# Kernel tuning notes

Measured on AMD Instinct MI355X. Metric: run time of the kernel, lower is better.

## Reference

```python
import jax, jax.numpy as jnp
import numpy as np

B, N, D = 8, 2048, 768
H = 12
HD = D // H
W = 16          # window_size
HOP = 8         # hop_size
GB = N // 2 + 1   # global freq bins = 1025
LB = W // 2 + 1   # local freq bins = 9
NW = (N - W) // HOP + 1  # num windows = 255
EPS_LN = 1e-5


def setup_inputs() -> dict:
    key = jax.random.key(0)
    ks = jax.random.split(key, 12)
    s = 0.02
    return {
        "x": jax.random.normal(ks[0], (B, N, D), dtype=jnp.float32),
        "base_filter_global": jnp.ones((H, GB, 1), jnp.float32),
        "base_filter_local": jnp.ones((H, LB, 1), jnp.float32),
        "modrelu_bias_global": jnp.full((H, GB, 1), -0.1, jnp.float32),
        "modrelu_bias_local": jnp.full((H, LB, 1), -0.1, jnp.float32),
        "w1g": jax.random.normal(ks[1], (D, D), jnp.float32) * s,
        "b1g": jnp.zeros((D,), jnp.float32),
        "w2g": jax.random.normal(ks[2], (D, H * GB), jnp.float32) * s,
        "b2g": jnp.zeros((H * GB,), jnp.float32),
        "w1l": jax.random.normal(ks[3], (D, D), jnp.float32) * s,
        "b1l": jnp.zeros((D,), jnp.float32),
        "w2l": jax.random.normal(ks[4], (D, H * LB), jnp.float32) * s,
        "b2l": jnp.zeros((H * LB,), jnp.float32),
        "fusion_w": jax.random.normal(ks[5], (2,), jnp.float32) * 0.5,
        "ln_gamma": jnp.ones((D,), jnp.float32),
        "ln_beta": jnp.zeros((D,), jnp.float32),
    }


def _modrelu(z, bias):
    # modReLU: ReLU(|z| + b) * z / |z|  (|z| clamped at 1e-6 in denominator)
    a = jnp.abs(z)
    return z * (jax.nn.relu(a + bias) / jnp.maximum(a, 1e-6))


def _hann(w):
    # torch.hann_window default (periodic=True)
    n = jnp.arange(w, dtype=jnp.float32)
    return 0.5 * (1.0 - jnp.cos(2.0 * jnp.pi * n / w))


def reference(x, base_filter_global, base_filter_local, modrelu_bias_global,
              modrelu_bias_local, w1g, b1g, w2g, b2g, w1l, b1l, w2l, b2l,
              fusion_w, ln_gamma, ln_beta):
    b, n, d = x.shape
    x_heads = x.reshape(b, n, H, HD).transpose(0, 2, 1, 3)  # (B,H,N,hd)

    # ---- global branch ----
    Fg = jnp.fft.rfft(x_heads, axis=2, norm='ortho')  # (B,H,GB,hd) complex
    ctx = x.mean(axis=1)  # (B,D)
    mg = jnp.tanh(jax.nn.gelu(ctx @ w1g + b1g, approximate=False) @ w2g + b2g)
    mg = mg.reshape(b, H, GB, 1)
    Fg = Fg * (base_filter_global[None] + mg)
    Fg = _modrelu(Fg, modrelu_bias_global[None])
    x_global = jnp.fft.irfft(Fg, n=n, axis=2, norm='ortho')  # (B,H,N,hd)

    # ---- local (STFT) branch ----
    idx = jnp.arange(NW)[:, None] * HOP + jnp.arange(W)[None, :]  # (NW,W)
    x_win = x_heads[:, :, idx, :]  # (B,H,NW,W,hd)
    w = _hann(W)[None, None, None, :, None]
    x_win = x_win * w
    Fl = jnp.fft.rfft(x_win, axis=3, norm='ortho')  # (B,H,NW,LB,hd)
    ml = jnp.tanh(jax.nn.gelu(ctx @ w1l + b1l, approximate=False) @ w2l + b2l)
    ml = ml.reshape(b, H, 1, LB, 1)
    Fl = Fl * (base_filter_local[None, :, None] + ml)
    Fl = _modrelu(Fl, modrelu_bias_local[None, :, None])
    x_lwin = jnp.fft.irfft(Fl, n=W, axis=3, norm='ortho') * w  # (B,H,NW,W,hd)

    # vectorized overlap-add
    flat_idx = idx.reshape(-1)  # (NW*W,)
    x_local = jnp.zeros((b, H, n, HD), x.dtype).at[:, :, flat_idx, :].add(
        x_lwin.reshape(b, H, NW * W, HD))

    # ---- fuse + residual + layernorm ----
    fused = x_global * fusion_w[0] + x_local * fusion_w[1]  # Linear(2,1,bias=False)
    x_out = fused.transpose(0, 2, 1, 3).reshape(b, n, d)
    y = x + x_out  # dropout is identity at p=0 / eval
    mu = y.mean(axis=-1, keepdims=True)
    var = y.var(axis=-1, keepdims=True)
    return (y - mu) / jnp.sqrt(var + EPS_LN) * ln_gamma + ln_beta
```

## Files before the change

kernel.cpp:

```cpp
#include <hip/hip_runtime.h>
#include <math.h>

#define B_  8
#define N_  2048
#define D_  768
#define H_  12
#define HD_ 64
#define GB_ 1025
#define LB_ 9
#define NW_ 255

#define CBX(i) ((i) + ((i) >> 4))
#define TWX(i) ((i) + ((i) >> 4))

#define C1_ 0.92387953251128674f
#define S1_ 0.38268343236508978f
#define R2_ 0.70710678118654752f

#define FBF(i,k,wr,wi) { const float ar=yr[i],ai=yi[i],br=yr[k],bi=yi[k]; \
  yr[i]=ar+br; yi[i]=ai+bi; const float dr=ar-br, di=ai-bi; \
  yr[k]=fmaf(dr,wr,-(di*(wi))); yi[k]=fmaf(dr,wi,di*(wr)); }
#define FBF1(i,k) { const float ar=yr[i],ai=yi[i],br=yr[k],bi=yi[k]; \
  yr[i]=ar+br; yi[i]=ai+bi; yr[k]=ar-br; yi[k]=ai-bi; }
#define FBFmi(i,k) { const float ar=yr[i],ai=yi[i],br=yr[k],bi=yi[k]; \
  yr[i]=ar+br; yi[i]=ai+bi; yr[k]=ai-bi; yi[k]=br-ar; }

#define IBF(i,k,wr,wi) { const float br=yr[k],bi=yi[k]; \
  const float tr=fmaf(br,wr,-(bi*(wi))), ti=fmaf(br,wi,bi*(wr)); \
  yr[k]=yr[i]-tr; yi[k]=yi[i]-ti; yr[i]+=tr; yi[i]+=ti; }
#define IBF1(i,k) { const float tr=yr[k], ti=yi[k]; \
  yr[k]=yr[i]-tr; yi[k]=yi[i]-ti; yr[i]+=tr; yi[i]+=ti; }
#define IBFpi(i,k) { const float tr=-yi[k], ti=yr[k]; \
  yr[k]=yr[i]-tr; yi[k]=yi[i]-ti; yr[i]+=tr; yi[i]+=ti; }

__device__ __forceinline__ float2 cmulf(float2 a, float2 b) {
  return make_float2(fmaf(a.x, b.x, -(a.y*b.y)), fmaf(a.x, b.y, a.y*b.x));
}
__device__ __forceinline__ float2 csqf(float2 a){ return make_float2(fmaf(a.x,a.x,-(a.y*a.y)), 2.0f*a.x*a.y); }

__device__ __forceinline__ float4 dadd(float4 a, float4 b){ return make_float4(a.x+b.x,a.y+b.y,a.z+b.z,a.w+b.w); }
__device__ __forceinline__ float4 dsub(float4 a, float4 b){ return make_float4(a.x-b.x,a.y-b.y,a.z-b.z,a.w-b.w); }
__device__ __forceinline__ float4 dmul(float4 a, float2 w){
  return make_float4(fmaf(a.x,w.x,-(a.y*w.y)), fmaf(a.x,w.y,a.y*w.x),
                     fmaf(a.z,w.x,-(a.w*w.y)), fmaf(a.z,w.y,a.w*w.x));
}
__device__ __forceinline__ float4 dmulc(float4 a, float2 w){
  return make_float4(fmaf(a.x,w.x,a.y*w.y), fmaf(a.y,w.x,-(a.x*w.y)),
                     fmaf(a.z,w.x,a.w*w.y), fmaf(a.w,w.x,-(a.z*w.y)));
}
__device__ __forceinline__ float4 dmuli(float4 a){
  return make_float4(a.y, -a.x, a.w, -a.z);
}
__device__ __forceinline__ float4 dmulpi(float4 a){
  return make_float4(-a.y, a.x, -a.w, a.z);
}

__device__ __forceinline__ void mr2(float& ar, float& ai, float filt, float bias){
  ar *= filt; ai *= filt;
  const float a = __builtin_amdgcn_sqrtf(fmaf(ar,ar,ai*ai));
  const float s = fmaxf(a + bias, 0.0f) * __builtin_amdgcn_rcpf(fmaxf(a, 1e-6f));
  ar *= s; ai *= s;
}
__device__ __forceinline__ void mr1(float& v, float filt, float bias){
  v *= filt;
  const float a = fabsf(v);
  v *= fmaxf(a + bias, 0.0f) * __builtin_amdgcn_rcpf(fmaxf(a, 1e-6f));
}

template<int S, int L>
__device__ __forceinline__ void fft_trip_fwd(float4* cb, const float2* tw, int j) {
  const int r    = j & (S-1);
  const int base = r + ((j >> L) << (L+3));
  float4 v[8];
  #pragma unroll
  for (int k = 0; k < 8; ++k) v[k] = cb[CBX(base + S*k)];
  const float2 w = tw[TWX(r * (256/S))];
  const float2 c8 = make_float2(R2_, -R2_);
  float2 W1[4];
  W1[0] = w;
  W1[1] = cmulf(w, c8);
  W1[2] = make_float2(w.y, -w.x);
  W1[3] = make_float2(W1[1].y, -W1[1].x);
  #pragma unroll
  for (int k = 0; k < 4; ++k) {
    const float4 u = v[k], t = v[k+4];
    v[k]   = dadd(u, t);
    v[k+4] = dmul(dsub(u, t), W1[k]);
  }
  const float2 w2  = csqf(w);
  const float2 w2i = make_float2(w2.y, -w2.x);
  {
    float4 d;
    d = dsub(v[0], v[2]); v[0] = dadd(v[0], v[2]); v[2] = dmul(d, w2);
    d = dsub(v[1], v[3]); v[1] = dadd(v[1], v[3]); v[3] = dmul(d, w2i);
    d = dsub(v[4], v[6]); v[4] = dadd(v[4], v[6]); v[6] = dmul(d, w2);
    d = dsub(v[5], v[7]); v[5] = dadd(v[5], v[7]); v[7] = dmul(d, w2i);
  }
  const float2 w4 = csqf(w2);
  #pragma unroll
  for (int k = 0; k < 8; k += 2) {
    const float4 d = dsub(v[k], v[k+1]);
    v[k]   = dadd(v[k], v[k+1]);
    v[k+1] = dmul(d, w4);
  }
  #pragma unroll
  for (int k = 0; k < 8; ++k) cb[CBX(base + S*k)] = v[k];
}

__device__ __forceinline__ void fft_trip4_fwd(float4* cb, int j) {
  const int base = j << 3;
  float4 v[8];
  #pragma unroll
  for (int k = 0; k < 8; ++k) v[k] = cb[CBX(base + k)];
  float4 d;
  d = dsub(v[0], v[2]); v[0] = dadd(v[0], v[2]); v[2] = d;
  d = dsub(v[1], v[3]); v[1] = dadd(v[1], v[3]); v[3] = dmuli(d);
  d = dsub(v[4], v[6]); v[4] = dadd(v[4], v[6]); v[6] = d;
  d = dsub(v[5], v[7]); v[5] = dadd(v[5], v[7]); v[7] = dmuli(d);
  #pragma unroll
  for (int k = 0; k < 8; k += 2) {
    d = dsub(v[k], v[k+1]);
    v[k]   = dadd(v[k], v[k+1]);
    v[k+1] = d;
  }
  #pragma unroll
  for (int k = 0; k < 8; ++k) cb[CBX(base + k)] = v[k];
}

__device__ __forceinline__ void fft_trip1_inv(float4* cb, int j) {
  const int base = j << 3;
  float4 v[8];
  #pragma unroll
  for (int k = 0; k < 8; ++k) v[k] = cb[CBX(base + k)];
  #pragma unroll
  for (int k = 0; k < 8; k += 2) {
    const float4 t = v[k+1];
    v[k+1] = dsub(v[k], t);
    v[k]   = dadd(v[k], t);
  }
  {
    float4 t;
    t = v[2];          v[2] = dsub(v[0], t); v[0] = dadd(v[0], t);
    t = dmulpi(v[3]);  v[3] = dsub(v[1], t); v[1] = dadd(v[1], t);
    t = v[6];          v[6] = dsub(v[4], t); v[4] = dadd(v[4], t);
    t = dmulpi(v[7]);  v[7] = dsub(v[5], t); v[5] = dadd(v[5], t);
  }
  #pragma unroll
  for (int k = 0; k < 8; ++k) cb[CBX(base + k)] = v[k];
}

template<int S, int L>
__device__ __forceinline__ void fft_trip_inv(float4* cb, const float2* tw, int j) {
  const int r    = j & (S-1);
  const int base = r + ((j >> L) << (L+3));
  float4 v[8];
  #pragma unroll
  for (int k = 0; k < 8; ++k) v[k] = cb[CBX(base + S*k)];
  const float2 w  = tw[TWX(r * (256/S))];
  const float2 w2 = csqf(w);
  const float2 w4 = csqf(w2);
  #pragma unroll
  for (int k = 0; k < 8; k += 2) {
    const float4 t = dmulc(v[k+1], w4);
    v[k+1] = dsub(v[k], t);
    v[k]   = dadd(v[k], t);
  }
  {
    float4 t;
    t = dmulc(v[2], w2);          v[2] = dsub(v[0], t); v[0] = dadd(v[0], t);
    t = dmulpi(dmulc(v[3], w2));  v[3] = dsub(v[1], t); v[1] = dadd(v[1], t);
    t = dmulc(v[6], w2);          v[6] = dsub(v[4], t); v[4] = dadd(v[4], t);
    t = dmulpi(dmulc(v[7], w2));  v[7] = dsub(v[5], t); v[5] = dadd(v[5], t);
  }
  const float2 c8 = make_float2(R2_, -R2_);
  float2 W1[4];
  W1[0] = w;
  W1[1] = cmulf(w, c8);
  W1[2] = make_float2(w.y, -w.x);
  W1[3] = make_float2(W1[1].y, -W1[1].x);
  #pragma unroll
  for (int k = 0; k < 4; ++k) {
    const float4 t = dmulc(v[k+4], W1[k]);
    v[k+4] = dsub(v[k], t);
    v[k]   = dadd(v[k], t);
  }
  #pragma unroll
  for (int k = 0; k < 8; ++k) cb[CBX(base + S*k)] = v[k];
}

template<int HALF>
__device__ __forceinline__ void local_path(const float4* cb, const float* lf, const float* lb,
                                           int tid, float* w1a, float* w2a) {
  const float HWIN[16] = {0.0f, 0.038060233744356624f, 0.14644660940672624f, 0.30865828381745508f,
                          0.5f, 0.69134171618254492f, 0.85355339059327376f, 0.96193976625564337f,
                          1.0f, 0.96193976625564337f, 0.85355339059327376f, 0.69134171618254492f,
                          0.5f, 0.30865828381745508f, 0.14644660940672624f, 0.038060233744356624f};
  if (tid < NW_) {
    float yr[16], yi[16];
    #pragma unroll
    for (int t = 0; t < 16; ++t) {
      const float4 v = cb[CBX(tid*8 + t)];
      yr[t] = (HALF ? v.z : v.x) * HWIN[t];
      yi[t] = (HALF ? v.w : v.y) * HWIN[t];
    }
    FBF1(0,8); FBF(1,9,C1_,-S1_); FBF(2,10,R2_,-R2_); FBF(3,11,S1_,-C1_);
    FBFmi(4,12); FBF(5,13,-S1_,-C1_); FBF(6,14,-R2_,-R2_); FBF(7,15,-C1_,-S1_);
    FBF1(0,4); FBF(1,5,R2_,-R2_); FBFmi(2,6); FBF(3,7,-R2_,-R2_);
    FBF1(8,12); FBF(9,13,R2_,-R2_); FBFmi(10,14); FBF(11,15,-R2_,-R2_);
    FBF1(0,2); FBFmi(1,3); FBF1(4,6); FBFmi(5,7);
    FBF1(8,10); FBFmi(9,11); FBF1(12,14); FBFmi(13,15);
    FBF1(0,1); FBF1(2,3); FBF1(4,5); FBF1(6,7);
    FBF1(8,9); FBF1(10,11); FBF1(12,13); FBF1(14,15);
    {
      const int IA[9] = {0,8,4,12,2,10,6,14,1};
      const int IB[9] = {0,15,7,11,3,13,5,9,1};
      #pragma unroll
      for (int l = 0; l <= 8; ++l) {
        const int ia = IA[l], ib = IB[l];
        const float Zar=yr[ia], Zai=yi[ia], Zbr=yr[ib], Zbi=yi[ib];
        float f1r = 0.125f*(Zar+Zbr), f1i = 0.125f*(Zai-Zbi);
        float f2r = 0.125f*(Zai+Zbi), f2i = 0.125f*(Zbr-Zar);
        const float ft = lf[l], bs = lb[l];
        mr2(f1r, f1i, ft, bs);
        mr2(f2r, f2i, ft, bs);
        yr[ia] = f1r - f2i; yi[ia] = f1i + f2r;
        if (l >= 1 && l <= 7) { yr[ib] = f1r + f2i; yi[ib] = f2r - f1i; }
      }
    }
    IBF1(0,1); IBF1(2,3); IBF1(4,5); IBF1(6,7);
    IBF1(8,9); IBF1(10,11); IBF1(12,13); IBF1(14,15);
    IBF1(0,2); IBFpi(1,3); IBF1(4,6); IBFpi(5,7);
    IBF1(8,10); IBFpi(9,11); IBF1(12,14); IBFpi(13,15);
    IBF1(0,4); IBF(1,5,R2_,R2_); IBFpi(2,6); IBF(3,7,-R2_,R2_);
    IBF1(8,12); IBF(9,13,R2_,R2_); IBFpi(10,14); IBF(11,15,-R2_,R2_);
    IBF1(0,8); IBF(1,9,C1_,S1_); IBF(2,10,R2_,R2_); IBF(3,11,S1_,C1_);
    IBFpi(4,12); IBF(5,13,-S1_,C1_); IBF(6,14,-R2_,R2_); IBF(7,15,-C1_,S1_);
    #pragma unroll
    for (int t = 0; t < 16; ++t) {
      const float q = 0.25f * HWIN[t];
      w1a[t] = yr[t] * q;
      w2a[t] = yi[t] * q;
    }
  } else {
    #pragma unroll
    for (int t = 0; t < 16; ++t) { w1a[t] = 0.0f; w2a[t] = 0.0f; }
  }
}

__device__ __forceinline__ void combine_oa(const float* w1a, const float* w2a,
                                           const float (*t1)[8], const float (*t2)[8],
                                           int lane, int wvi, float* r1, float* r2) {
  #pragma unroll
  for (int s = 0; s < 8; ++s) {
    float p1 = __shfl_up(w1a[s+8], 1, 64);
    float p2 = __shfl_up(w2a[s+8], 1, 64);
    if (lane == 0) {
      p1 = wvi ? t1[wvi-1][s] : 0.0f;
      p2 = wvi ? t2[wvi-1][s] : 0.0f;
    }
    r1[s] = w1a[s] + p1;
    r2[s] = w2a[s] + p2;
  }
}

__global__ __launch_bounds__(256) void k_ctx(const float* __restrict__ x,
                                             float* __restrict__ ctx) {
  const int b = blockIdx.x;
  const int nc = blockIdx.y;
  const int tid = threadIdx.x;
  const int n0 = nc * 64;
  for (int c = tid; c < D_; c += 256) {
    float s = 0.0f;
    #pragma unroll 4
    for (int n = 0; n < 64; ++n)
      s += x[((size_t)(b*N_ + n0 + n))*D_ + c];
    atomicAdd(&ctx[b*D_ + c], s);
  }
}

__global__ __launch_bounds__(256) void k_mlp1(
    const float* __restrict__ ctx,
    const float* __restrict__ w1g, const float* __restrict__ b1g,
    const float* __restrict__ w1l, const float* __restrict__ b1l,
    float* __restrict__ h1g, float* __restrict__ h1l) {
  __shared__ float hs[D_];
  __shared__ float red[4][16][5];
  const int tid = threadIdx.x;
  const bool isl = (blockIdx.y != 0);
  const int bb = blockIdx.z;
  const float* w1 = isl ? w1l : w1g;
  const float* b1 = isl ? b1l : b1g;
  float*       h1 = isl ? h1l : h1g;
  const int j0 = (int)blockIdx.x * 64;

  for (int i = tid; i < D_; i += 256) hs[i] = ctx[bb*D_ + i] * (1.0f/(float)N_);
  __syncthreads();

  const int jg    = tid & 15;
  const int slice = tid >> 4;
  const int j     = j0 + jg*4;
  float acc[4] = {};
  {
    const float4* w14 = (const float4*)w1;
    const int jc = j >> 2;
    const int i0 = slice*48;
    #pragma unroll 4
    for (int ii = 0; ii < 48; ++ii) {
      const int i = i0 + ii;
      const float4 w = w14[(size_t)i*192 + jc];
      const float hv = hs[i];
      acc[0] = fmaf(hv, w.x, acc[0]);
      acc[1] = fmaf(hv, w.y, acc[1]);
      acc[2] = fmaf(hv, w.z, acc[2]);
      acc[3] = fmaf(hv, w.w, acc[3]);
    }
  }
  #pragma unroll
  for (int q = 0; q < 4; ++q) {
    float v = acc[q];
    v += __shfl_xor(v, 16, 64);
    v += __shfl_xor(v, 32, 64);
    acc[q] = v;
  }
  const int wv = tid >> 6;
  if ((tid & 63) < 16) {
    #pragma unroll
    for (int q = 0; q < 4; ++q)
      red[wv][jg][q] = acc[q];
  }
  __syncthreads();
  if (tid < 64) {
    const int jg2 = tid >> 2;
    const int q   = tid & 3;
    const int jo  = j0 + jg2*4 + q;
    const float sum = red[0][jg2][q] + red[1][jg2][q]
                    + red[2][jg2][q] + red[3][jg2][q];
    const float v = sum + b1[jo];
    h1[(size_t)bb*D_ + jo] = 0.5f * v * (1.0f + erff(v * 0.70710678118654752f));
  }
}

__global__ __launch_bounds__(256) void k_mlp2(
    const float* __restrict__ h1g, const float* __restrict__ h1l,
    const float* __restrict__ w2g, const float* __restrict__ b2g,
    const float* __restrict__ w2l, const float* __restrict__ b2l,
    float* __restrict__ mg, float* __restrict__ ml) {
  __shared__ float hs[B_*D_];
  __shared__ float red[4][16][33];
  const int tid = threadIdx.x;
  const bool isg = (blockIdx.x < 193);
  const float* h1 = isg ? h1g : h1l;
  const float* w2 = isg ? w2g : w2l;
  const float* b2 = isg ? b2g : b2l;
  float*       mo = isg ? mg  : ml;
  const int Jmax = isg ? (H_*GB_) : (H_*LB_);
  const int j0   = isg ? (int)blockIdx.x*64 : ((int)blockIdx.x-193)*64;

  for (int i = tid; i < B_*D_; i += 256) hs[i] = h1[i];
  __syncthreads();

  const int jg    = tid & 15;
  const int slice = tid >> 4;
  const int j     = j0 + jg*4;
  float acc[8][4] = {};
  if (j < Jmax) {
    const float4* w24 = (const float4*)w2;
    const int jc   = j >> 2;
    const int rowq = Jmax >> 2;
    const int i0   = slice*48;
    #pragma unroll 4
    for (int ii = 0; ii < 48; ++ii) {
      const int i = i0 + ii;
      const float4 w = w24[(size_t)i*rowq + jc];
      #pragma unroll
      for (int b = 0; b < 8; ++b) {
        const float hv = hs[b*D_ + i];
        acc[b][0] = fmaf(hv, w.x, acc[b][0]);
        acc[b][1] = fmaf(hv, w.y, acc[b][1]);
        acc[b][2] = fmaf(hv, w.z, acc[b][2]);
        acc[b][3] = fmaf(hv, w.w, acc[b][3]);
      }
    }
  }
  #pragma unroll
  for (int b = 0; b < 8; ++b) {
    #pragma unroll
    for (int q = 0; q < 4; ++q) {
      float v = acc[b][q];
      v += __shfl_xor(v, 16, 64);
      v += __shfl_xor(v, 32, 64);
      acc[b][q] = v;
    }
  }
  const int wv = tid >> 6;
  if ((tid & 63) < 16) {
    #pragma unroll
    for (int b = 0; b < 8; ++b)
      #pragma unroll
      for (int q = 0; q < 4; ++q)
        red[wv][jg][b*4+q] = acc[b][q];
  }
  __syncthreads();
  for (int s = tid; s < 512; s += 256) {
    const int jg2 = s >> 5;
    const int v2  = s & 31;
    const int b   = v2 >> 2, q = v2 & 3;
    const int jo  = j0 + jg2*4 + q;
    if (jo < Jmax) {
      const float sum = red[0][jg2][v2] + red[1][jg2][v2]
                      + red[2][jg2][v2] + red[3][jg2][v2];
      mo[(size_t)b*Jmax + jo] = tanhf(sum + b2[jo]);
    }
  }
}

__global__ __launch_bounds__(256) void k_spectral(
    const float* __restrict__ x,
    const float* __restrict__ bfg, const float* __restrict__ bfl,
    const float* __restrict__ mbg, const float* __restrict__ mbl,
    const float* __restrict__ mg,  const float* __restrict__ ml,
    const float* __restrict__ fw,  float* __restrict__ fused) {
  __shared__ float4 cb[N_ + (N_>>4)];
  __shared__ float2 tw[256 + 16];
  __shared__ float  t1b[2][4][8], t2b[2][4][8];
  __shared__ float  lf[LB_], lb[LB_];

  const int tid = threadIdx.x;
  const int id  = blockIdx.x;
  const int v_  = (id & 7) * 192 + (id >> 3);
  const int dq  = v_ & 15;
  const int bh  = v_ >> 4;
  const int h   = bh % H_;
  const int b   = bh / H_;
  const int d   = dq * 4;
  const int c   = h*HD_ + d;
  const int cg  = bh*16 + dq;

  {
    float s_, c_;
    sincospif(-(float)tid * (1.0f/1024.0f), &s_, &c_);
    tw[TWX(tid)] = make_float2(c_, s_);
  }
  if (tid < LB_) {
    lf[tid] = bfl[h*LB_ + tid] + ml[(size_t)b*(H_*LB_) + h*LB_ + tid];
    lb[tid] = mbl[h*LB_ + tid];
  }
  const float* xp = &x[((size_t)(b*N_))*D_ + c];
  for (int n = tid; n < N_; n += 256) {
    cb[CBX(n)] = *(const float4*)&xp[(size_t)n*D_];
  }
  __syncthreads();

  const int lane = tid & 63, wvi = tid >> 6;
  float r1[8], r2[8], r3[8], r4[8];
  {
    float w1a[16], w2a[16];
    local_path<0>(cb, lf, lb, tid, w1a, w2a);
    if (lane == 63 && tid < NW_) {
      #pragma unroll
      for (int s = 0; s < 8; ++s) { t1b[0][wvi][s] = w1a[8+s]; t2b[0][wvi][s] = w2a[8+s]; }
    }
    __syncthreads();
    combine_oa(w1a, w2a, t1b[0], t2b[0], lane, wvi, r1, r2);
  }
  {
    float w1a[16], w2a[16];
    local_path<1>(cb, lf, lb, tid, w1a, w2a);
    if (lane == 63 && tid < NW_) {
      #pragma unroll
      for (int s = 0; s < 8; ++s) { t1b[1][wvi][s] = w1a[8+s]; t2b[1][wvi][s] = w2a[8+s]; }
    }
    __syncthreads();
    combine_oa(w1a, w2a, t1b[1], t2b[1], lane, wvi, r3, r4);
  }

  fft_trip_fwd<256,8>(cb, tw, tid); __syncthreads();
  fft_trip_fwd< 32,5>(cb, tw, tid); __syncthreads();
  fft_trip_fwd<  4,2>(cb, tw, tid); __syncthreads();
  fft_trip4_fwd(cb, tid);           __syncthreads();

  const float fsc = 0.022097086912079610f;
  {
    const float* mgp = mg + (size_t)b*(H_*GB_) + h*GB_;
    const float* bfp = bfg + h*GB_;
    const float* mbp = mbg + h*GB_;
    const int kb = (tid & 192) + (int)(__brev((unsigned)(tid & 63)) >> 26);
    #pragma unroll
    for (int t = 0; t < 4; ++t) {
      const int k = kb + 256*t;
      if (k == 0) {
        float4 Z0 = cb[CBX(0)], Zn = cb[CBX(1)];
        const float f0t = bfp[0] + mgp[0],     b0 = mbp[0];
        const float fnt = bfp[1024] + mgp[1024], bn = mbp[1024];
        float a0 = Z0.x*fsc, a1 = Z0.y*fsc, a2 = Z0.z*fsc, a3 = Z0.w*fsc;
        mr1(a0, f0t, b0); mr1(a1, f0t, b0); mr1(a2, f0t, b0); mr1(a3, f0t, b0);
        cb[CBX(0)] = make_float4(a0, a1, a2, a3);
        float n0v = Zn.x*fsc, n1v = Zn.y*fsc, n2v = Zn.z*fsc, n3v = Zn.w*fsc;
        mr1(n0v, fnt, bn); mr1(n1v, fnt, bn); mr1(n2v, fnt, bn); mr1(n3v, fnt, bn);
        cb[CBX(1)] = make_float4(n0v, n1v, n2v, n3v);
      } else {
        const int ik  = (int)(__brev((unsigned)k) >> 21);
        const int imk = (int)(__brev((unsigned)(2048 - k)) >> 21);
        const float4 Za = cb[CBX(ik)], Zb = cb[CBX(imk)];
        const float hs_ = 0.5f * fsc;
        const float filt = bfp[k] + mgp[k], bias = mbp[k];
        float f1r = (Za.x + Zb.x) * hs_, f1i = (Za.y - Zb.y) * hs_;
        float f2r = (Za.y + Zb.y) * hs_, f2i = (Zb.x - Za.x) * hs_;
        mr2(f1r, f1i, filt, bias);
        mr2(f2r, f2i, filt, bias);
        float g1r = (Za.z + Zb.z) * hs_, g1i = (Za.w - Zb.w) * hs_;
        float g2r = (Za.w + Zb.w) * hs_, g2i = (Zb.z - Za.z) * hs_;
        mr2(g1r, g1i, filt, bias);
        mr2(g2r, g2i, filt, bias);
        cb[CBX(ik)]  = make_float4(f1r - f2i, f1i + f2r, g1r - g2i, g1i + g2r);
        cb[CBX(imk)] = make_float4(f1r + f2i, f2r - f1i, g1r + g2i, g2r - g1i);
      }
    }
  }
  __syncthreads();

  fft_trip1_inv(cb, tid);           __syncthreads();
  fft_trip_inv<  4,2>(cb, tw, tid); __syncthreads();
  fft_trip_inv< 32,5>(cb, tw, tid); __syncthreads();
  fft_trip_inv<256,8>(cb, tw, tid); __syncthreads();

  const float fw1v = fw[1];
  const float fwg  = fw[0] * fsc;
  float4* fo = (float4*)fused + (size_t)cg * N_;
  const int n0 = tid * 8;
  #pragma unroll
  for (int s = 0; s < 8; ++s) {
    const float4 g  = cb[CBX(n0 + s)];
    const float4 xv = *(const float4*)&xp[(size_t)(n0 + s)*D_];
    fo[n0 + s] = make_float4(xv.x + fwg * g.x + fw1v * r1[s],
                             xv.y + fwg * g.y + fw1v * r2[s],
                             xv.z + fwg * g.z + fw1v * r3[s],
                             xv.w + fwg * g.w + fw1v * r4[s]);
  }
}

__global__ __launch_bounds__(256) void k_ln(const float* __restrict__ fused,
                                            const float* __restrict__ gamma,
                                            const float* __restrict__ beta,
                                            float* __restrict__ out) {
  __shared__ float yt[16*776];
  __shared__ float mus[16], rsd[16];
  const int bi = blockIdx.x;
  const int b  = bi >> 7;
  const int n0 = (bi & 127) * 16;
  const int tid = threadIdx.x;

  {
    const float4* fu4 = (const float4*)fused;
    for (int i = tid; i < 16*192; i += 256) {
      const int cgl = i >> 4, rn = i & 15;
      const float4 g = fu4[((size_t)(b*192 + cgl))*N_ + n0 + rn];
      float* yp = &yt[rn*776 + cgl*4];
      yp[0] = g.x; yp[1] = g.y; yp[2] = g.z; yp[3] = g.w;
    }
  }
  __syncthreads();
  const int nn = tid >> 4, cl = tid & 15;
  float s1 = 0.0f, s2 = 0.0f;
  for (int c = cl; c < D_; c += 16) {
    const float v = yt[nn*776 + c];
    s1 += v; s2 += v*v;
  }
  #pragma unroll
  for (int m = 8; m >= 1; m >>= 1) {
    s1 += __shfl_xor(s1, m, 16);
    s2 += __shfl_xor(s2, m, 16);
  }
  if (cl == 0) {
    const float mu  = s1 * (1.0f/(float)D_);
    const float var = s2 * (1.0f/(float)D_) - mu*mu;
    mus[nn] = mu;
    rsd[nn] = rsqrtf(var + 1e-5f);
  }
  __syncthreads();
  {
    float4* o4 = (float4*)(out + ((size_t)(b*N_ + n0))*D_);
    const float4* g4 = (const float4*)gamma;
    const float4* be4 = (const float4*)beta;
    for (int i = tid; i < 16*D_/4; i += 256) {
      const int nn2 = i / 192, r = i - nn2*192;
      const float mu = mus[nn2], rs = rsd[nn2];
      const float4 gm = g4[r], bt = be4[r];
      const float* yp = &yt[nn2*776 + r*4];
      float4 o;
      o.x = (yp[0] - mu) * rs * gm.x + bt.x;
      o.y = (yp[1] - mu) * rs * gm.y + bt.y;
      o.z = (yp[2] - mu) * rs * gm.z + bt.z;
      o.w = (yp[3] - mu) * rs * gm.w + bt.w;
      o4[i] = o;
    }
  }
}

extern "C" void kernel_launch(void* const* d_in, const int* in_sizes, int n_in,
                              void* d_out, int out_size, void* d_ws, size_t ws_size,
                              hipStream_t stream) {
  const float* x   = (const float*)d_in[0];
  const float* bfg = (const float*)d_in[1];
  const float* bfl = (const float*)d_in[2];
  const float* mbg = (const float*)d_in[3];
  const float* mbl = (const float*)d_in[4];
  const float* w1g = (const float*)d_in[5];
  const float* b1g = (const float*)d_in[6];
  const float* w2g = (const float*)d_in[7];
  const float* b2g = (const float*)d_in[8];
  const float* w1l = (const float*)d_in[9];
  const float* b1l = (const float*)d_in[10];
  const float* w2l = (const float*)d_in[11];
  const float* b2l = (const float*)d_in[12];
  const float* fw  = (const float*)d_in[13];
  const float* gam = (const float*)d_in[14];
  const float* bet = (const float*)d_in[15];
  float* out = (float*)d_out;

  float* ws    = (float*)d_ws;
  float* ctx   = ws;
  float* h1g   = ws + 6144;
  float* h1l   = ws + 12288;
  float* mg    = ws + 18432;
  float* ml    = ws + 116832;
  float* fused = ws + 117696;

  hipMemsetAsync(ctx, 0, (size_t)B_*D_*sizeof(float), stream);
  k_ctx<<<dim3(B_, 32), 256, 0, stream>>>(x, ctx);
  k_mlp1<<<dim3(12, 2, 8), 256, 0, stream>>>(ctx, w1g, b1g, w1l, b1l, h1g, h1l);
  k_mlp2<<<195, 256, 0, stream>>>(h1g, h1l, w2g, b2g, w2l, b2l, mg, ml);
  k_spectral<<<B_*H_*16, 256, 0, stream>>>(x, bfg, bfl, mbg, mbl, mg, ml, fw, fused);
  k_ln<<<B_*N_/16, 256, 0, stream>>>(fused, gam, bet, out);
}
```

Measured before the change: 280.2 us.

## Merge ctx reduction and MLP kernels into one cooperative kernel with grid syncs

Replaces the memset, the ctx reduction and the two MLP kernels with a single cooperative kernel of 256 blocks that uses grid.sync between stages. The atomic ctx accumulation becomes per-chunk partial sums stored in the fused buffer and reduced during the first MLP stage. This is meant to remove three launch gaps and the atomics, at the cost of grid-wide barriers and a fixed 256-block grid that must all be co-resident.

Result: slower. 403.4 us (+44.0%).

```diff
diff --git a/kernel.cpp b/kernel.cpp
--- a/kernel.cpp
+++ b/kernel.cpp
@@ -1,4 +1,5 @@
 #include <hip/hip_runtime.h>
+#include <hip/hip_cooperative_groups.h>
 #include <math.h>
 
 #define B_  8
@@ -263,153 +264,164 @@
   }
 }
 
-__global__ __launch_bounds__(256) void k_ctx(const float* __restrict__ x,
-                                             float* __restrict__ ctx) {
-  const int b = blockIdx.x;
-  const int nc = blockIdx.y;
-  const int tid = threadIdx.x;
-  const int n0 = nc * 64;
-  for (int c = tid; c < D_; c += 256) {
-    float s = 0.0f;
-    #pragma unroll 4
-    for (int n = 0; n < 64; ++n)
-      s += x[((size_t)(b*N_ + n0 + n))*D_ + c];
-    atomicAdd(&ctx[b*D_ + c], s);
-  }
-}
-
-__global__ __launch_bounds__(256) void k_mlp1(
-    const float* __restrict__ ctx,
+__global__ __launch_bounds__(256) void k_mlpchain(
+    const float* __restrict__ x,
     const float* __restrict__ w1g, const float* __restrict__ b1g,
     const float* __restrict__ w1l, const float* __restrict__ b1l,
-    float* __restrict__ h1g, float* __restrict__ h1l) {
-  __shared__ float hs[D_];
-  __shared__ float red[4][16][5];
-  const int tid = threadIdx.x;
-  const bool isl = (blockIdx.y != 0);
-  const int bb = blockIdx.z;
-  const float* w1 = isl ? w1l : w1g;
-  const float* b1 = isl ? b1l : b1g;
-  float*       h1 = isl ? h1l : h1g;
-  const int j0 = (int)blockIdx.x * 64;
-
-  for (int i = tid; i < D_; i += 256) hs[i] = ctx[bb*D_ + i] * (1.0f/(float)N_);
-  __syncthreads();
-
-  const int jg    = tid & 15;
-  const int slice = tid >> 4;
-  const int j     = j0 + jg*4;
-  float acc[4] = {};
-  {
-    const float4* w14 = (const float4*)w1;
-    const int jc = j >> 2;
-    const int i0 = slice*48;
-    #pragma unroll 4
-    for (int ii = 0; ii < 48; ++ii) {
-      const int i = i0 + ii;
-      const float4 w = w14[(size_t)i*192 + jc];
-      const float hv = hs[i];
-      acc[0] = fmaf(hv, w.x, acc[0]);
-      acc[1] = fmaf(hv, w.y, acc[1]);
-      acc[2] = fmaf(hv, w.z, acc[2]);
-      acc[3] = fmaf(hv, w.w, acc[3]);
-    }
-  }
-  #pragma unroll
-  for (int q = 0; q < 4; ++q) {
-    float v = acc[q];
-    v += __shfl_xor(v, 16, 64);
-    v += __shfl_xor(v, 32, 64);
-    acc[q] = v;
-  }
-  const int wv = tid >> 6;
-  if ((tid & 63) < 16) {
-    #pragma unroll
-    for (int q = 0; q < 4; ++q)
-      red[wv][jg][q] = acc[q];
-  }
-  __syncthreads();
-  if (tid < 64) {
-    const int jg2 = tid >> 2;
-    const int q   = tid & 3;
-    const int jo  = j0 + jg2*4 + q;
-    const float sum = red[0][jg2][q] + red[1][jg2][q]
-                    + red[2][jg2][q] + red[3][jg2][q];
-    const float v = sum + b1[jo];
-    h1[(size_t)bb*D_ + jo] = 0.5f * v * (1.0f + erff(v * 0.70710678118654752f));
-  }
-}
-
-__global__ __launch_bounds__(256) void k_mlp2(
-    const float* __restrict__ h1g, const float* __restrict__ h1l,
     const float* __restrict__ w2g, const float* __restrict__ b2g,
     const float* __restrict__ w2l, const float* __restrict__ b2l,
+    float* __restrict__ ctxp, float* __restrict__ h1g, float* __restrict__ h1l,
     float* __restrict__ mg, float* __restrict__ ml) {
+  cooperative_groups::grid_group grid = cooperative_groups::this_grid();
   __shared__ float hs[B_*D_];
   __shared__ float red[4][16][33];
   const int tid = threadIdx.x;
-  const bool isg = (blockIdx.x < 193);
-  const float* h1 = isg ? h1g : h1l;
-  const float* w2 = isg ? w2g : w2l;
-  const float* b2 = isg ? b2g : b2l;
-  float*       mo = isg ? mg  : ml;
-  const int Jmax = isg ? (H_*GB_) : (H_*LB_);
-  const int j0   = isg ? (int)blockIdx.x*64 : ((int)blockIdx.x-193)*64;
-
-  for (int i = tid; i < B_*D_; i += 256) hs[i] = h1[i];
-  __syncthreads();
-
-  const int jg    = tid & 15;
-  const int slice = tid >> 4;
-  const int j     = j0 + jg*4;
-  float acc[8][4] = {};
-  if (j < Jmax) {
-    const float4* w24 = (const float4*)w2;
-    const int jc   = j >> 2;
-    const int rowq = Jmax >> 2;
-    const int i0   = slice*48;
-    #pragma unroll 4
-    for (int ii = 0; ii < 48; ++ii) {
-      const int i = i0 + ii;
-      const float4 w = w24[(size_t)i*rowq + jc];
-      #pragma unroll
-      for (int b = 0; b < 8; ++b) {
-        const float hv = hs[b*D_ + i];
-        acc[b][0] = fmaf(hv, w.x, acc[b][0]);
-        acc[b][1] = fmaf(hv, w.y, acc[b][1]);
-        acc[b][2] = fmaf(hv, w.z, acc[b][2]);
-        acc[b][3] = fmaf(hv, w.w, acc[b][3]);
+  const int bid = blockIdx.x;
+
+  {
+    const int b  = bid >> 5;
+    const int nc = bid & 31;
+    const int n0 = nc * 64;
+    for (int c = tid; c < D_; c += 256) {
+      float s = 0.0f;
+      #pragma unroll 4
+      for (int n = 0; n < 64; ++n)
+        s += x[((size_t)(b*N_ + n0 + n))*D_ + c];
+      ctxp[(size_t)(nc*B_ + b)*D_ + c] = s;
+    }
+  }
+  __threadfence();
+  grid.sync();
+
+  if (bid < 192) {
+    const int jx   = bid % 12;
+    const int rest = bid / 12;
+    const bool isl = (rest & 1) != 0;
+    const int bb   = rest >> 1;
+    const float* w1 = isl ? w1l : w1g;
+    const float* b1 = isl ? b1l : b1g;
+    float*       h1 = isl ? h1l : h1g;
+    const int j0 = jx * 64;
+
+    for (int i = tid; i < D_; i += 256) {
+      float s = 0.0f;
+      #pragma unroll 8
+      for (int p = 0; p < 32; ++p)
+        s += ctxp[(size_t)p*(B_*D_) + bb*D_ + i];
+      hs[i] = s * (1.0f/(float)N_);
+    }
+    __syncthreads();
+
+    const int jg    = tid & 15;
+    const int slice = tid >> 4;
+    const int j     = j0 + jg*4;
+    float acc[4] = {};
+    {
+      const float4* w14 = (const float4*)w1;
+      const int jc = j >> 2;
+      const int i0 = slice*48;
+      #pragma unroll 4
+      for (int ii = 0; ii < 48; ++ii) {
+        const int i = i0 + ii;
+        const float4 w = w14[(size_t)i*192 + jc];
+        const float hv = hs[i];
+        acc[0] = fmaf(hv, w.x, acc[0]);
+        acc[1] = fmaf(hv, w.y, acc[1]);
+        acc[2] = fmaf(hv, w.z, acc[2]);
+        acc[3] = fmaf(hv, w.w, acc[3]);
       }
     }
-  }
-  #pragma unroll
-  for (int b = 0; b < 8; ++b) {
     #pragma unroll
     for (int q = 0; q < 4; ++q) {
-      float v = acc[b][q];
+      float v = acc[q];
       v += __shfl_xor(v, 16, 64);
       v += __shfl_xor(v, 32, 64);
-      acc[b][q] = v;
-    }
-  }
-  const int wv = tid >> 6;
-  if ((tid & 63) < 16) {
-    #pragma unroll
-    for (int b = 0; b < 8; ++b)
+      acc[q] = v;
+    }
+    const int wv = tid >> 6;
+    if ((tid & 63) < 16) {
       #pragma unroll
       for (int q = 0; q < 4; ++q)
-        red[wv][jg][b*4+q] = acc[b][q];
-  }
-  __syncthreads();
-  for (int s = tid; s < 512; s += 256) {
-    const int jg2 = s >> 5;
-    const int v2  = s & 31;
-    const int b   = v2 >> 2, q = v2 & 3;
-    const int jo  = j0 + jg2*4 + q;
-    if (jo < Jmax) {
-      const float sum = red[0][jg2][v2] + red[1][jg2][v2]
-                      + red[2][jg2][v2] + red[3][jg2][v2];
-      mo[(size_t)b*Jmax + jo] = tanhf(sum + b2[jo]);
+        red[wv][jg][q] = acc[q];
+    }
+    __syncthreads();
+    if (tid < 64) {
+      const int jg2 = tid >> 2;
+      const int q   = tid & 3;
+      const int jo  = j0 + jg2*4 + q;
+      const float sum = red[0][jg2][q] + red[1][jg2][q]
+                      + red[2][jg2][q] + red[3][jg2][q];
+      const float v = sum + b1[jo];
+      h1[(size_t)bb*D_ + jo] = 0.5f * v * (1.0f + erff(v * 0.70710678118654752f));
+    }
+  }
+  __threadfence();
+  grid.sync();
+
+  if (bid < 195) {
+    const bool isg = (bid < 193);
+    const float* h1 = isg ? h1g : h1l;
+    const float* w2 = isg ? w2g : w2l;
+    const float* b2 = isg ? b2g : b2l;
+    float*       mo = isg ? mg  : ml;
+    const int Jmax = isg ? (H_*GB_) : (H_*LB_);
+    const int j0   = isg ? bid*64 : (bid-193)*64;
+
+    for (int i = tid; i < B_*D_; i += 256) hs[i] = h1[i];
+    __syncthreads();
+
+    const int jg    = tid & 15;
+    const int slice = tid >> 4;
+    const int j     = j0 + jg*4;
+    float acc[8][4] = {};
+    if (j < Jmax) {
+      const float4* w24 = (const float4*)w2;
+      const int jc   = j >> 2;
+      const int rowq = Jmax >> 2;
+      const int i0   = slice*48;
+      #pragma unroll 4
+      for (int ii = 0; ii < 48; ++ii) {
+        const int i = i0 + ii;
+        const float4 w = w24[(size_t)i*rowq + jc];
+        #pragma unroll
+        for (int b = 0; b < 8; ++b) {
+          const float hv = hs[b*D_ + i];
+          acc[b][0] = fmaf(hv, w.x, acc[b][0]);
+          acc[b][1] = fmaf(hv, w.y, acc[b][1]);
+          acc[b][2] = fmaf(hv, w.z, acc[b][2]);
+          acc[b][3] = fmaf(hv, w.w, acc[b][3]);
+        }
+      }
+    }
+    #pragma unroll
+    for (int b = 0; b < 8; ++b) {
+      #pragma unroll
+      for (int q = 0; q < 4; ++q) {
+        float v = acc[b][q];
+        v += __shfl_xor(v, 16, 64);
+        v += __shfl_xor(v, 32, 64);
+        acc[b][q] = v;
+      }
+    }
+    const int wv = tid >> 6;
+    if ((tid & 63) < 16) {
+      #pragma unroll
+      for (int b = 0; b < 8; ++b)
+        #pragma unroll
+        for (int q = 0; q < 4; ++q)
+          red[wv][jg][b*4+q] = acc[b][q];
+    }
+    __syncthreads();
+    for (int s = tid; s < 512; s += 256) {
+      const int jg2 = s >> 5;
+      const int v2  = s & 31;
+      const int b   = v2 >> 2, q = v2 & 3;
+      const int jo  = j0 + jg2*4 + q;
+      if (jo < Jmax) {
+        const float sum = red[0][jg2][v2] + red[1][jg2][v2]
+                        + red[2][jg2][v2] + red[3][jg2][v2];
+        mo[(size_t)b*Jmax + jo] = tanhf(sum + b2[jo]);
+      }
     }
   }
 }
@@ -619,17 +631,21 @@
   float* out = (float*)d_out;
 
   float* ws    = (float*)d_ws;
-  float* ctx   = ws;
   float* h1g   = ws + 6144;
   float* h1l   = ws + 12288;
   float* mg    = ws + 18432;
   float* ml    = ws + 116832;
   float* fused = ws + 117696;
-
-  hipMemsetAsync(ctx, 0, (size_t)B_*D_*sizeof(float), stream);
-  k_ctx<<<dim3(B_, 32), 256, 0, stream>>>(x, ctx);
-  k_mlp1<<<dim3(12, 2, 8), 256, 0, stream>>>(ctx, w1g, b1g, w1l, b1l, h1g, h1l);
-  k_mlp2<<<195, 256, 0, stream>>>(h1g, h1l, w2g, b2g, w2l, b2l, mg, ml);
+  float* ctxp  = fused;
+
+  {
+    void* args[] = { (void*)&x,
+                     (void*)&w1g, (void*)&b1g, (void*)&w1l, (void*)&b1l,
+                     (void*)&w2g, (void*)&b2g, (void*)&w2l, (void*)&b2l,
+                     (void*)&ctxp, (void*)&h1g, (void*)&h1l, (void*)&mg, (void*)&ml };
+    hipLaunchCooperativeKernel((const void*)k_mlpchain, dim3(256), dim3(256),
+                               args, 0, stream);
+  }
   k_spectral<<<B_*H_*16, 256, 0, stream>>>(x, bfg, bfl, mbg, mbl, mg, ml, fw, fused);
   k_ln<<<B_*N_/16, 256, 0, stream>>>(fused, gam, bet, out);
 }
```
